# Kernel optimization log

Measured on AMD Instinct MI355X. Metric: run time of the kernel, lower is better.

## Reference

```python
import jax, jax.numpy as jnp
import numpy as np

EPS = 1e-5   # torch.nn.BatchNorm default eps
K = 27       # 3x3x3 octree conv kernel size


def _octree_conv(x, neigh, W):
    """Octree sparse 3x3x3 conv: per kernel offset, gather neighbor features
    and matmul. x: [N, C], neigh: [N, K] int32, W: [K, C, D] -> [N, D].
    Loop over the 27 fixed offsets avoids materializing the [N, 27, C] gather."""
    out = jnp.zeros((x.shape[0], W.shape[2]), dtype=x.dtype)
    for k in range(K):
        out = out + x[neigh[:, k]] @ W[k]
    return out


def _bn(x, gamma, beta):
    # BatchNorm1d in training mode: normalize over the node dimension.
    m = jnp.mean(x, axis=0)
    v = jnp.var(x, axis=0)
    return (x - m) * jax.lax.rsqrt(v + EPS) * gamma + beta


def setup_inputs() -> dict:
    key = jax.random.key(0)
    ks = jax.random.split(key, 5)
    N, Cin, Cout = 500000, 128, 256  # bottleneck=1 => channelb == Cout
    data = jax.random.normal(ks[0], (N, Cin), dtype=jnp.float32)
    neigh = jax.random.randint(ks[1], (N, K), 0, N, dtype=jnp.int32)
    Wa = jax.random.normal(ks[2], (K, Cin, Cout), dtype=jnp.float32) / np.sqrt(K * Cin)
    Wb = jax.random.normal(ks[3], (K, Cout, Cout), dtype=jnp.float32) / np.sqrt(K * Cout)
    W1 = jax.random.normal(ks[4], (Cin, Cout), dtype=jnp.float32) / np.sqrt(Cin)
    return {
        "data": data, "neigh": neigh, "depth": 5,
        "Wa": Wa, "ga": jnp.ones(Cout), "ba": jnp.zeros(Cout),
        "Wb": Wb, "gb": jnp.ones(Cout), "bb": jnp.zeros(Cout),
        "W1": W1, "gs": jnp.ones(Cout), "bs": jnp.zeros(Cout),
    }


def reference(data, neigh, depth, Wa, ga, ba, Wb, gb, bb, W1, gs, bs):
    # stride == 1 => no maxpool, depth unchanged (depth unused beyond routing).
    conv1 = jax.nn.relu(_bn(_octree_conv(data, neigh, Wa), ga, ba))  # Conv3x3+BN+ReLU
    conv2 = _bn(_octree_conv(conv1, neigh, Wb), gb, bb)              # Conv3x3+BN
    shortcut = _bn(data @ W1, gs, bs)                                # Conv1x1+BN (Cin != Cout)
    return jax.nn.relu(conv2 + shortcut)
```

## Files before the change

kernel.cpp:

```cpp
#include <hip/hip_runtime.h>
#include <hip/hip_bf16.h>
#include <stdint.h>

typedef __attribute__((ext_vector_type(8))) short bf16x8;
typedef __attribute__((ext_vector_type(4))) float f32x4;

#define AS1(p) ((const __attribute__((address_space(1))) void*)(p))
#define AS3(p) ((__attribute__((address_space(3))) void*)(p))

__device__ __forceinline__ unsigned short f2bf(float f) {
    union { float f; unsigned u; } v; v.f = f;
    unsigned r = v.u + 0x7fffu + ((v.u >> 16) & 1u);
    return (unsigned short)(r >> 16);
}
__device__ __forceinline__ float bf2f(unsigned short h) {
    union { unsigned u; float f; } v; v.u = ((unsigned)h) << 16;
    return v.f;
}

template<int CIN, bool GATHER, bool OUT_BF16>
__global__ __launch_bounds__(512, 2) void conv_kernel(
    const unsigned short* __restrict__ in,
    const int* __restrict__ neigh,
    const unsigned short* __restrict__ Wt,
    void* __restrict__ outp,
    float* __restrict__ stats,
    int N, int NK)
{
    constexpr int KT = 64;
    constexpr int NKT = CIN / KT;
    __shared__ unsigned short Alds[3][128 * KT];
    __shared__ unsigned short Blds[2][256 * KT];
    __shared__ int nlds[GATHER ? 128 * 27 : 8];

    const int tid  = threadIdx.x;
    const int lane = tid & 63;
    const int wid  = tid >> 6;
    const int wr   = wid >> 2, wc = wid & 3;
    const int brow = blockIdx.x * 128;

    if (GATHER) {
        for (int s = tid; s < 128 * 27; s += 512) {
            int r = s / 27, kk = s - r * 27;
            int grow = brow + r;
            nlds[s] = (grow < N) ? neigh[(size_t)grow * 27 + kk] : 0;
        }
        __syncthreads();
    }

    const int T = NK * NKT;

    auto stageA = [&](int t) {
        const int k = t / NKT, kt = t - (t / NKT) * NKT;
        char* dst = (char*)&Alds[t % 3][0];
        #pragma unroll
        for (int i = 0; i < 2; ++i) {
            int s = i * 512 + tid;
            int r = s >> 3, seg = s & 7;
            int g = GATHER ? nlds[r * 27 + k] : (brow + r);
            const char* src = (const char*)in + ((size_t)g * CIN + kt * KT) * 2
                            + ((seg ^ (r & 7)) * 16);
            __builtin_amdgcn_global_load_lds(AS1(src),
                AS3(dst + (i * 512 + wid * 64) * 16), 16, 0, 0);
        }
    };
    auto stageB = [&](int t) {
        const int k = t / NKT, kt = t - (t / NKT) * NKT;
        char* dst = (char*)&Blds[t & 1][0];
        #pragma unroll
        for (int i = 0; i < 4; ++i) {
            int s = i * 512 + tid;
            int c = s >> 3, seg = s & 7;
            const char* src = (const char*)Wt
                + (((size_t)k * 256 + c) * CIN + kt * KT) * 2
                + ((seg ^ (c & 7)) * 16);
            __builtin_amdgcn_global_load_lds(AS1(src),
                AS3(dst + (i * 512 + wid * 64) * 16), 16, 0, 0);
        }
    };

    f32x4 acc[4][4] = {};

    stageA(0);
    stageB(0);
    if (T > 1) stageA(1);

    for (int t = 0; t < T; ++t) {
        if (t + 1 < T) stageB(t + 1);
        if (t + 2 < T) stageA(t + 2);
        __builtin_amdgcn_sched_barrier(0);
        if (t + 2 < T)      asm volatile("s_waitcnt vmcnt(8)" ::: "memory");
        else if (t + 1 < T) asm volatile("s_waitcnt vmcnt(6)" ::: "memory");
        else                asm volatile("s_waitcnt vmcnt(0)" ::: "memory");
        __builtin_amdgcn_sched_barrier(0);
        __builtin_amdgcn_s_barrier();
        __builtin_amdgcn_sched_barrier(0);

        const char* Ab = (const char*)&Alds[t % 3][0];
        const char* Bb = (const char*)&Blds[t & 1][0];
        bf16x8 bfr[4][2];
        #pragma unroll
        for (int n = 0; n < 4; ++n)
            #pragma unroll
            for (int kk = 0; kk < 2; ++kk) {
                int c = wc * 64 + n * 16 + (lane & 15);
                int byte = (c * 128 + kk * 64 + ((lane >> 4) * 16)) ^ ((c & 7) << 4);
                bfr[n][kk] = *(const bf16x8*)(Bb + byte);
            }
        #pragma unroll
        for (int m = 0; m < 4; ++m) {
            bf16x8 af[2];
            #pragma unroll
            for (int kk = 0; kk < 2; ++kk) {
                int r = wr * 64 + m * 16 + (lane & 15);
                int byte = (r * 128 + kk * 64 + ((lane >> 4) * 16)) ^ ((r & 7) << 4);
                af[kk] = *(const bf16x8*)(Ab + byte);
            }
            __builtin_amdgcn_s_setprio(1);
            #pragma unroll
            for (int n = 0; n < 4; ++n) {
                acc[m][n] = __builtin_amdgcn_mfma_f32_16x16x32_bf16(af[0], bfr[n][0], acc[m][n], 0, 0, 0);
                acc[m][n] = __builtin_amdgcn_mfma_f32_16x16x32_bf16(af[1], bfr[n][1], acc[m][n], 0, 0, 0);
            }
            __builtin_amdgcn_s_setprio(0);
        }
        __builtin_amdgcn_sched_barrier(0);
        __builtin_amdgcn_s_barrier();
        __builtin_amdgcn_sched_barrier(0);
    }

    #pragma unroll
    for (int n = 0; n < 4; ++n) {
        float s = 0.f, q = 0.f;
        #pragma unroll
        for (int m = 0; m < 4; ++m)
            #pragma unroll
            for (int j = 0; j < 4; ++j) {
                int row = brow + wr * 64 + m * 16 + ((lane >> 4) * 4) + j;
                float v = (row < N) ? acc[m][n][j] : 0.f;
                s += v; q += v * v;
            }
        s += __shfl_xor(s, 16); s += __shfl_xor(s, 32);
        q += __shfl_xor(q, 16); q += __shfl_xor(q, 32);
        if (lane < 16) {
            int col = wc * 64 + n * 16 + lane;
            atomicAdd(&stats[col], s);
            atomicAdd(&stats[256 + col], q);
        }
    }
    #pragma unroll
    for (int m = 0; m < 4; ++m) {
        #pragma unroll
        for (int j = 0; j < 4; ++j) {
            int row = brow + wr * 64 + m * 16 + ((lane >> 4) * 4) + j;
            if (row < N) {
                #pragma unroll
                for (int n = 0; n < 4; ++n) {
                    int col = wc * 64 + n * 16 + (lane & 15);
                    float v = acc[m][n][j];
                    if (OUT_BF16)
                        ((unsigned short*)outp)[(size_t)row * 256 + col] = f2bf(v);
                    else
                        __builtin_nontemporal_store(v, &((float*)outp)[(size_t)row * 256 + col]);
                }
            }
        }
    }
}

__global__ void cast_x_kernel(const float* __restrict__ x, unsigned short* __restrict__ xb, size_t n8) {
    size_t stride = (size_t)gridDim.x * blockDim.x;
    for (size_t i = (size_t)blockIdx.x * blockDim.x + threadIdx.x; i < n8; i += stride) {
        const float4* p = (const float4*)(x + i * 8);
        float4 f0 = p[0], f1 = p[1];
        unsigned short o[8];
        o[0] = f2bf(f0.x); o[1] = f2bf(f0.y); o[2] = f2bf(f0.z); o[3] = f2bf(f0.w);
        o[4] = f2bf(f1.x); o[5] = f2bf(f1.y); o[6] = f2bf(f1.z); o[7] = f2bf(f1.w);
        *(uint4*)(xb + i * 8) = *(uint4*)o;
    }
}

__global__ void cast_wT_kernel(const float* __restrict__ w, unsigned short* __restrict__ wt,
                               int NK, int CI, int CO) {
    int total = NK * CI * CO;
    int stride = gridDim.x * blockDim.x;
    for (int id = blockIdx.x * blockDim.x + threadIdx.x; id < total; id += stride) {
        int ci = id % CI;
        int t  = id / CI;
        int co = t % CO;
        int k  = t / CO;
        wt[id] = f2bf(w[((size_t)k * CI + ci) * CO + co]);
    }
}

__global__ void finalize_kernel(const float* __restrict__ stats, const float* __restrict__ gamma,
                                const float* __restrict__ beta, float* __restrict__ coef, float invN) {
    int c = threadIdx.x;
    float mean = stats[c] * invN;
    float var  = fmaxf(stats[256 + c] * invN - mean * mean, 0.f);
    float a = gamma[c] * rsqrtf(var + 1e-5f);
    coef[c] = a;
    coef[256 + c] = beta[c] - mean * a;
}

__global__ void bn_relu_kernel(unsigned short* __restrict__ buf, const float* __restrict__ coef, size_t n8) {
    size_t stride = (size_t)gridDim.x * blockDim.x;
    for (size_t i = (size_t)blockIdx.x * blockDim.x + threadIdx.x; i < n8; i += stride) {
        uint4 v = *(uint4*)(buf + i * 8);
        unsigned short* h = (unsigned short*)&v;
        int cb = (int)((i * 8) & 255);
        #pragma unroll
        for (int j = 0; j < 8; ++j) {
            float f = bf2f(h[j]) * coef[cb + j] + coef[256 + cb + j];
            h[j] = f2bf(fmaxf(f, 0.f));
        }
        *(uint4*)(buf + i * 8) = v;
    }
}

__global__ void final_kernel(float* __restrict__ out, const unsigned short* __restrict__ sc,
                             const float* __restrict__ c2, const float* __restrict__ cs, size_t n4) {
    size_t stride = (size_t)gridDim.x * blockDim.x;
    for (size_t i = (size_t)blockIdx.x * blockDim.x + threadIdx.x; i < n4; i += stride) {
        float4 o = *(float4*)(out + i * 4);
        ushort4 s4 = *(const ushort4*)(sc + i * 4);
        int cb = (int)((i * 4) & 255);
        float r;
        r = o.x * c2[cb + 0] + c2[256 + cb + 0] + bf2f(s4.x) * cs[cb + 0] + cs[256 + cb + 0]; o.x = fmaxf(r, 0.f);
        r = o.y * c2[cb + 1] + c2[256 + cb + 1] + bf2f(s4.y) * cs[cb + 1] + cs[256 + cb + 1]; o.y = fmaxf(r, 0.f);
        r = o.z * c2[cb + 2] + c2[256 + cb + 2] + bf2f(s4.z) * cs[cb + 2] + cs[256 + cb + 2]; o.z = fmaxf(r, 0.f);
        r = o.w * c2[cb + 3] + c2[256 + cb + 3] + bf2f(s4.w) * cs[cb + 3] + cs[256 + cb + 3]; o.w = fmaxf(r, 0.f);
        *(float4*)(out + i * 4) = o;
    }
}

extern "C" void kernel_launch(void* const* d_in, const int* in_sizes, int n_in,
                              void* d_out, int out_size, void* d_ws, size_t ws_size,
                              hipStream_t stream) {
    const float* data = (const float*)d_in[0];
    const int*   neigh = (const int*)d_in[1];
    const float* Wa = (const float*)d_in[3];
    const float* ga = (const float*)d_in[4];
    const float* ba = (const float*)d_in[5];
    const float* Wb = (const float*)d_in[6];
    const float* gb = (const float*)d_in[7];
    const float* bb = (const float*)d_in[8];
    const float* W1 = (const float*)d_in[9];
    const float* gs = (const float*)d_in[10];
    const float* bs = (const float*)d_in[11];

    const int N = in_sizes[0] / 128;
    const int nblk = (N + 127) / 128;
    const int Npad = nblk * 128;

    char* ws = (char*)d_ws;
    float* stats1 = (float*)(ws + 0);
    float* stats2 = (float*)(ws + 2048);
    float* statss = (float*)(ws + 4096);
    float* c1     = (float*)(ws + 6144);
    float* c2     = (float*)(ws + 8192);
    float* cs     = (float*)(ws + 10240);
    unsigned short* WaT = (unsigned short*)(ws + 16384);
    unsigned short* WbT = WaT + (size_t)27 * 256 * 128;
    unsigned short* W1T = WbT + (size_t)27 * 256 * 256;
    unsigned short* Xb  = W1T + (size_t)256 * 128;
    unsigned short* buf1 = Xb + (size_t)Npad * 128;

    hipMemsetAsync(d_ws, 0, 16384, stream);
    if (Npad > N)
        hipMemsetAsync(Xb + (size_t)N * 128, 0, (size_t)(Npad - N) * 128 * 2, stream);

    cast_x_kernel<<<2048, 256, 0, stream>>>(data, Xb, (size_t)N * 128 / 8);
    cast_wT_kernel<<<1024, 256, 0, stream>>>(Wa, WaT, 27, 128, 256);
    cast_wT_kernel<<<1024, 256, 0, stream>>>(Wb, WbT, 27, 256, 256);
    cast_wT_kernel<<<64, 256, 0, stream>>>(W1, W1T, 1, 128, 256);

    conv_kernel<128, true, true><<<nblk, 512, 0, stream>>>(Xb, neigh, WaT, buf1, stats1, N, 27);
    finalize_kernel<<<1, 256, 0, stream>>>(stats1, ga, ba, c1, 1.0f / N);
    bn_relu_kernel<<<2048, 256, 0, stream>>>(buf1, c1, (size_t)N * 256 / 8);
    conv_kernel<256, true, false><<<nblk, 512, 0, stream>>>(buf1, neigh, WbT, d_out, stats2, N, 27);
    conv_kernel<128, false, true><<<nblk, 512, 0, stream>>>(Xb, nullptr, W1T, buf1, statss, N, 1);
    finalize_kernel<<<1, 256, 0, stream>>>(stats2, gb, bb, c2, 1.0f / N);
    finalize_kernel<<<1, 256, 0, stream>>>(statss, gs, bs, cs, 1.0f / N);
    final_kernel<<<2048, 256, 0, stream>>>((float*)d_out, buf1, c2, cs, (size_t)N * 256 / 4);
}
```

Measured before the change: 4.747 ms.

## Load weight fragments directly from global memory and drop B LDS staging

Weight tiles are no longer staged through shared memory. Each wave now loads its B fragments straight from global memory into registers, and the A gather buffer goes from triple to double buffering. This shrinks LDS use a lot, and launch bounds are raised to target 4 blocks per CU for higher occupancy. The cost is that B loads now sit on the critical path every iteration with only a shallow prefetch, and the waitcnt placement leaves little latency hiding. Register pressure also rises under the tighter launch bound.

```diff
diff --git a/kernel.cpp b/kernel.cpp
--- a/kernel.cpp
+++ b/kernel.cpp
@@ -19,7 +19,7 @@
 }
 
 template<int CIN, bool GATHER, bool OUT_BF16>
-__global__ __launch_bounds__(512, 2) void conv_kernel(
+__global__ __launch_bounds__(512, 4) void conv_kernel(
     const unsigned short* __restrict__ in,
     const int* __restrict__ neigh,
     const unsigned short* __restrict__ Wt,
@@ -29,8 +29,7 @@
 {
     constexpr int KT = 64;
     constexpr int NKT = CIN / KT;
-    __shared__ unsigned short Alds[3][128 * KT];
-    __shared__ unsigned short Blds[2][256 * KT];
+    __shared__ unsigned short Alds[2][128 * KT];
     __shared__ int nlds[GATHER ? 128 * 27 : 8];
 
     const int tid  = threadIdx.x;
@@ -52,7 +51,7 @@
 
     auto stageA = [&](int t) {
         const int k = t / NKT, kt = t - (t / NKT) * NKT;
-        char* dst = (char*)&Alds[t % 3][0];
+        char* dst = (char*)&Alds[t & 1][0];
         #pragma unroll
         for (int i = 0; i < 2; ++i) {
             int s = i * 512 + tid;
@@ -64,49 +63,35 @@
                 AS3(dst + (i * 512 + wid * 64) * 16), 16, 0, 0);
         }
     };
-    auto stageB = [&](int t) {
+
+    int boff[4];
+    #pragma unroll
+    for (int n = 0; n < 4; ++n)
+        boff[n] = (wc * 64 + n * 16 + (lane & 15)) * (CIN * 2) + ((lane >> 4) * 16);
+
+    f32x4 acc[4][4] = {};
+
+    stageA(0);
+    for (int t = 0; t < T; ++t) {
         const int k = t / NKT, kt = t - (t / NKT) * NKT;
-        char* dst = (char*)&Blds[t & 1][0];
-        #pragma unroll
-        for (int i = 0; i < 4; ++i) {
-            int s = i * 512 + tid;
-            int c = s >> 3, seg = s & 7;
-            const char* src = (const char*)Wt
-                + (((size_t)k * 256 + c) * CIN + kt * KT) * 2
-                + ((seg ^ (c & 7)) * 16);
-            __builtin_amdgcn_global_load_lds(AS1(src),
-                AS3(dst + (i * 512 + wid * 64) * 16), 16, 0, 0);
-        }
-    };
-
-    f32x4 acc[4][4] = {};
-
-    stageA(0);
-    stageB(0);
-    if (T > 1) stageA(1);
-
-    for (int t = 0; t < T; ++t) {
-        if (t + 1 < T) stageB(t + 1);
-        if (t + 2 < T) stageA(t + 2);
-        __builtin_amdgcn_sched_barrier(0);
-        if (t + 2 < T)      asm volatile("s_waitcnt vmcnt(8)" ::: "memory");
-        else if (t + 1 < T) asm volatile("s_waitcnt vmcnt(6)" ::: "memory");
-        else                asm volatile("s_waitcnt vmcnt(0)" ::: "memory");
+
+        const char* wb = (const char*)Wt + ((size_t)k * 256 * CIN) * 2 + kt * 128;
+        bf16x8 bfr[4][2];
+        #pragma unroll
+        for (int n = 0; n < 4; ++n) {
+            bfr[n][0] = *(const bf16x8*)(wb + boff[n]);
+            bfr[n][1] = *(const bf16x8*)(wb + boff[n] + 64);
+        }
+        __builtin_amdgcn_sched_barrier(0);
+        if (t + 1 < T) stageA(t + 1);
+        __builtin_amdgcn_sched_barrier(0);
+        if (t + 1 < T) asm volatile("s_waitcnt vmcnt(2)" ::: "memory");
+        else           asm volatile("s_waitcnt vmcnt(0)" ::: "memory");
         __builtin_amdgcn_sched_barrier(0);
         __builtin_amdgcn_s_barrier();
         __builtin_amdgcn_sched_barrier(0);
 
-        const char* Ab = (const char*)&Alds[t % 3][0];
-        const char* Bb = (const char*)&Blds[t & 1][0];
-        bf16x8 bfr[4][2];
-        #pragma unroll
-        for (int n = 0; n < 4; ++n)
-            #pragma unroll
-            for (int kk = 0; kk < 2; ++kk) {
-                int c = wc * 64 + n * 16 + (lane & 15);
-                int byte = (c * 128 + kk * 64 + ((lane >> 4) * 16)) ^ ((c & 7) << 4);
-                bfr[n][kk] = *(const bf16x8*)(Bb + byte);
-            }
+        const char* Ab = (const char*)&Alds[t & 1][0];
         #pragma unroll
         for (int m = 0; m < 4; ++m) {
             bf16x8 af[2];
```

Measured after the change: 6.177 ms. 30.1% more time.
